# Performance work log

Hardware: AMD Instinct MI355X
Metric: run time of the kernel (lower is better)

The kernel has to match this reference:

```python
import jax, jax.numpy as jnp
import numpy as np

H = 512      # hidden_size
Z = 128      # z_dim
E = 512      # embedding_dim
D = 2 * H + Z  # GRU hidden / decoder state dim = 1152
V = 32000    # output_size
BS = 256
N = 128      # encoder nodes per source


def setup_inputs() -> dict:
    key = jax.random.key(0)
    ks = jax.random.split(key, 24)
    s = 0.05
    inp = {
        "prev_y": jax.random.normal(ks[0], (BS, E), jnp.float32),
        "prev_h": jax.random.normal(ks[1], (BS, D), jnp.float32),
        "equ_enc": jax.random.normal(ks[2], (BS, N, H), jnp.float32),
        "sns_enc": jax.random.normal(ks[3], (BS, N, H), jnp.float32),
        "z_sample": jax.random.normal(ks[4], (BS, Z), jnp.float32),
        "equ_mask": jax.random.randint(ks[5], (BS, N), 0, 2) > 0,
        "sns_mask": jax.random.randint(ks[6], (BS, N), 0, 2) > 0,
        # Attention (equ): W1: HxH, W2: HxD, vt: 1xH (torch Linear weight = [out,in])
        "W1e": jax.random.normal(ks[7], (H, H), jnp.float32) * s,
        "W2e": jax.random.normal(ks[8], (H, D), jnp.float32) * s,
        "vte": jax.random.normal(ks[9], (1, H), jnp.float32) * s,
        "W1s": jax.random.normal(ks[10], (H, H), jnp.float32) * s,
        "W2s": jax.random.normal(ks[11], (H, D), jnp.float32) * s,
        "vts": jax.random.normal(ks[12], (1, H), jnp.float32) * s,
        "plan_W": jax.random.normal(ks[13], (2, D), jnp.float32) * s,
        "plan_b": jax.random.normal(ks[14], (2,), jnp.float32) * s,
        "Wc": jax.random.normal(ks[15], (H, E + H), jnp.float32) * s,
        "bc": jax.random.normal(ks[16], (H,), jnp.float32) * s,
        # GRU: input H -> hidden D
        "w_ih": jax.random.normal(ks[17], (3 * D, H), jnp.float32) * s,
        "w_hh": jax.random.normal(ks[18], (3 * D, D), jnp.float32) * s,
        "b_ih": jax.random.normal(ks[19], (3 * D,), jnp.float32) * s,
        "b_hh": jax.random.normal(ks[20], (3 * D,), jnp.float32) * s,
        "Wout": jax.random.normal(ks[21], (V, D), jnp.float32) * s,
        "bout": jax.random.normal(ks[22], (V,), jnp.float32) * s,
    }
    return inp


def _attn(h, enc, mask, W1, W2, vt):
    # enc: (b,n,H), h: (b,D)
    et = jnp.einsum('bnh,kh->bnk', enc, W1)          # (b,n,H)
    dt = (h @ W2.T)[:, None, :]                       # (b,1,H)
    u = jnp.einsum('bnh,h->bn', jnp.tanh(et + dt), vt[0])
    u = jnp.where(mask, -jnp.inf, u)
    return jax.nn.softmax(u, axis=-1)                 # (b,n)


def reference(prev_y, prev_h, equ_enc, sns_enc, z_sample, equ_mask, sns_mask,
              W1e, W2e, vte, W1s, W2s, vts, plan_W, plan_b, Wc, bc,
              w_ih, w_hh, b_ih, b_hh, Wout, bout):
    aw_e = _attn(prev_h, equ_enc, equ_mask, W1e, W2e, vte)
    ctx_e = jnp.einsum('bn,bnh->bh', aw_e, equ_enc)
    aw_s = _attn(prev_h, sns_enc, sns_mask, W1s, W2s, vts)
    ctx_s = jnp.einsum('bn,bnh->bh', aw_s, sns_enc)
    plan = jax.nn.softmax(prev_h @ plan_W.T + plan_b, axis=-1)  # (b,2)
    combine = jnp.stack([ctx_e, ctx_s], axis=1)                  # (b,2,H)
    context = jnp.einsum('bk,bkh->bh', plan, combine)
    y_ctx = jnp.concatenate([prev_y, context], axis=-1)          # (b,E+H)
    x = y_ctx @ Wc.T + bc                                        # (b,H)
    # single-step GRU (torch gate order: r, z, n)
    gx = x @ w_ih.T + b_ih                                       # (b,3D)
    gh = prev_h @ w_hh.T + b_hh
    Dh = prev_h.shape[-1]
    gx_r, gx_z, gx_n = gx[:, :Dh], gx[:, Dh:2*Dh], gx[:, 2*Dh:]
    gh_r, gh_z, gh_n = gh[:, :Dh], gh[:, Dh:2*Dh], gh[:, 2*Dh:]
    r = jax.nn.sigmoid(gx_r + gh_r)
    zg = jax.nn.sigmoid(gx_z + gh_z)
    n = jnp.tanh(gx_n + r * gh_n)
    h_new = (1.0 - zg) * n + zg * prev_h                          # (b,D)
    dec_output = (h_new @ Wout.T + bout)[:, None, :]              # (b,1,V)
    dec_hidden = h_new[None]                                      # (1,b,D)
    return dec_output, dec_hidden, plan
```

## Files before the change

kernel.cpp:

```cpp
#include <hip/hip_runtime.h>
#include <stdint.h>
#include <math.h>

#define BS_  256
#define NSEQ 128
#define HH   512
#define DD   1152
#define VV   32000
#define BN_  (BS_*NSEQ)

typedef float  f32x4  __attribute__((ext_vector_type(4)));
typedef __bf16 bf16x8 __attribute__((ext_vector_type(8)));

__device__ __forceinline__ f32x4 mfma16(bf16x8 a, bf16x8 b, f32x4 c) {
    return __builtin_amdgcn_mfma_f32_16x16x32_bf16(a, b, c, 0, 0, 0);
}

__device__ __forceinline__ bf16x8 pack8(f32x4 a, f32x4 b) {
    bf16x8 v;
    v[0] = (__bf16)a[0]; v[1] = (__bf16)a[1]; v[2] = (__bf16)a[2]; v[3] = (__bf16)a[3];
    v[4] = (__bf16)b[0]; v[5] = (__bf16)b[1]; v[6] = (__bf16)b[2]; v[7] = (__bf16)b[3];
    return v;
}

__device__ __forceinline__ float tanh_fast(float x) {
    float e = __expf(2.f * x);
    return 1.f - __fdividef(2.f, e + 1.f);
}

__global__ __launch_bounds__(256) void k_tile128(
    const float* __restrict__ A, const float* __restrict__ B,
    const float* __restrict__ bias, float* __restrict__ C,
    int K, int ldc)
{
    const int rb = blockIdx.x * 128;
    const int cb = blockIdx.y * 128;
    const int t = threadIdx.x;
    const int w = t >> 6, wr = w >> 1, wc = w & 1;
    const int lane = t & 63, g = lane >> 4, r = lane & 15;
    const int s_row = t >> 1, s_h = t & 1;

    __shared__ bf16x8 sm[2][2][512];

    const float* Ap = A + (size_t)(rb + s_row) * K + s_h * 16;
    const float* Bp = B + (size_t)(cb + s_row) * K + s_h * 16;

    const int kg0 = 2 * s_h, kg1 = 2 * s_h + 1;
    const int swz0 = kg0 * 128 + ((s_row & 112) | ((s_row ^ (kg0 << 2)) & 15));
    const int swz1 = kg1 * 128 + ((s_row & 112) | ((s_row ^ (kg1 << 2)) & 15));

    int ai[4], bi[4];
    #pragma unroll
    for (int i = 0; i < 4; ++i) {
        ai[i] = g * 128 + wr * 64 + i * 16 + ((r ^ (g << 2)) & 15);
        bi[i] = g * 128 + wc * 64 + i * 16 + ((r ^ (g << 2)) & 15);
    }

    const int KS = K >> 5;
    f32x4 pa0 = ((const f32x4*)Ap)[0], pa1 = ((const f32x4*)Ap)[1],
          pa2 = ((const f32x4*)Ap)[2], pa3 = ((const f32x4*)Ap)[3];
    f32x4 pb0 = ((const f32x4*)Bp)[0], pb1 = ((const f32x4*)Bp)[1],
          pb2 = ((const f32x4*)Bp)[2], pb3 = ((const f32x4*)Bp)[3];

    f32x4 acc[4][4];
    #pragma unroll
    for (int i = 0; i < 4; ++i)
        #pragma unroll
        for (int j = 0; j < 4; ++j) acc[i][j] = (f32x4){0.f, 0.f, 0.f, 0.f};

    for (int kb = 0; kb < KS; ++kb) {
        const int buf = kb & 1;
        sm[buf][0][swz0] = pack8(pa0, pa1);
        sm[buf][0][swz1] = pack8(pa2, pa3);
        sm[buf][1][swz0] = pack8(pb0, pb1);
        sm[buf][1][swz1] = pack8(pb2, pb3);
        __syncthreads();
        if (kb + 1 < KS) {
            const float* a2 = Ap + (kb + 1) * 32;
            const float* b2 = Bp + (kb + 1) * 32;
            pa0 = ((const f32x4*)a2)[0]; pa1 = ((const f32x4*)a2)[1];
            pa2 = ((const f32x4*)a2)[2]; pa3 = ((const f32x4*)a2)[3];
            pb0 = ((const f32x4*)b2)[0]; pb1 = ((const f32x4*)b2)[1];
            pb2 = ((const f32x4*)b2)[2]; pb3 = ((const f32x4*)b2)[3];
        }
        bf16x8 af[4], bfr[4];
        #pragma unroll
        for (int i = 0; i < 4; ++i) af[i]  = sm[buf][0][ai[i]];
        #pragma unroll
        for (int j = 0; j < 4; ++j) bfr[j] = sm[buf][1][bi[j]];
        #pragma unroll
        for (int i = 0; i < 4; ++i)
            #pragma unroll
            for (int j = 0; j < 4; ++j)
                acc[i][j] = mfma16(af[i], bfr[j], acc[i][j]);
    }

    #pragma unroll
    for (int j = 0; j < 4; ++j) {
        const int col = cb + wc * 64 + j * 16 + r;
        const float bv = bias ? bias[col] : 0.f;
        #pragma unroll
        for (int i = 0; i < 4; ++i) {
            #pragma unroll
            for (int q = 0; q < 4; ++q) {
                const int row = rb + wr * 64 + i * 16 + g * 4 + q;
                C[(size_t)row * ldc + col] = acc[i][j][q] + bv;
            }
        }
    }
}

__global__ __launch_bounds__(256) void k_vocab(
    const float* __restrict__ A, const float* __restrict__ B,
    const float* __restrict__ bias, float* __restrict__ C,
    int K, int ldc)
{
    const int L = blockIdx.x;
    const int p  = (L & 7) + ((L >> 4) << 3);
    const int rr = (L >> 3) & 1;
    if (p >= 250) return;
    const int rb = rr * 128;
    const int cb = p * 128;

    const int t = threadIdx.x;
    const int w = t >> 6, wr = w >> 1, wc = w & 1;
    const int lane = t & 63, g = lane >> 4, r = lane & 15;
    const int s_row = t >> 1, s_h = t & 1;

    __shared__ bf16x8 sm[2][2][512];

    const float* Ap = A + (size_t)(rb + s_row) * K + s_h * 16;
    const float* Bp = B + (size_t)(cb + s_row) * K + s_h * 16;

    const int kg0 = 2 * s_h, kg1 = 2 * s_h + 1;
    const int swz0 = kg0 * 128 + ((s_row & 112) | ((s_row ^ (kg0 << 2)) & 15));
    const int swz1 = kg1 * 128 + ((s_row & 112) | ((s_row ^ (kg1 << 2)) & 15));

    int ai[4], bi[4];
    #pragma unroll
    for (int i = 0; i < 4; ++i) {
        ai[i] = g * 128 + wr * 64 + i * 16 + ((r ^ (g << 2)) & 15);
        bi[i] = g * 128 + wc * 64 + i * 16 + ((r ^ (g << 2)) & 15);
    }

    const int KS = K >> 5;
    f32x4 pa0 = ((const f32x4*)Ap)[0], pa1 = ((const f32x4*)Ap)[1],
          pa2 = ((const f32x4*)Ap)[2], pa3 = ((const f32x4*)Ap)[3];
    f32x4 pb0 = ((const f32x4*)Bp)[0], pb1 = ((const f32x4*)Bp)[1],
          pb2 = ((const f32x4*)Bp)[2], pb3 = ((const f32x4*)Bp)[3];

    f32x4 acc[4][4];
    #pragma unroll
    for (int i = 0; i < 4; ++i)
        #pragma unroll
        for (int j = 0; j < 4; ++j) acc[i][j] = (f32x4){0.f, 0.f, 0.f, 0.f};

    for (int kb = 0; kb < KS; ++kb) {
        const int buf = kb & 1;
        sm[buf][0][swz0] = pack8(pa0, pa1);
        sm[buf][0][swz1] = pack8(pa2, pa3);
        sm[buf][1][swz0] = pack8(pb0, pb1);
        sm[buf][1][swz1] = pack8(pb2, pb3);
        __syncthreads();
        if (kb + 1 < KS) {
            const float* a2 = Ap + (kb + 1) * 32;
            const float* b2 = Bp + (kb + 1) * 32;
            pa0 = ((const f32x4*)a2)[0]; pa1 = ((const f32x4*)a2)[1];
            pa2 = ((const f32x4*)a2)[2]; pa3 = ((const f32x4*)a2)[3];
            pb0 = ((const f32x4*)b2)[0]; pb1 = ((const f32x4*)b2)[1];
            pb2 = ((const f32x4*)b2)[2]; pb3 = ((const f32x4*)b2)[3];
        }
        bf16x8 af[4], bfr[4];
        #pragma unroll
        for (int i = 0; i < 4; ++i) af[i]  = sm[buf][0][ai[i]];
        #pragma unroll
        for (int j = 0; j < 4; ++j) bfr[j] = sm[buf][1][bi[j]];
        #pragma unroll
        for (int i = 0; i < 4; ++i)
            #pragma unroll
            for (int j = 0; j < 4; ++j)
                acc[i][j] = mfma16(af[i], bfr[j], acc[i][j]);
    }

    #pragma unroll
    for (int j = 0; j < 4; ++j) {
        const int col = cb + wc * 64 + j * 16 + r;
        const float bv = bias[col];
        #pragma unroll
        for (int i = 0; i < 4; ++i) {
            #pragma unroll
            for (int q = 0; q < 4; ++q) {
                const int row = rb + wr * 64 + i * 16 + g * 4 + q;
                C[(size_t)row * ldc + col] = acc[i][j][q] + bv;
            }
        }
    }
}

__global__ __launch_bounds__(256) void k_prevh(
    const float* __restrict__ prev_h, const float* __restrict__ W2e,
    const float* __restrict__ W2s, const float* __restrict__ w_hh,
    const float* __restrict__ b_hh,
    float* __restrict__ dt_e, float* __restrict__ dt_s, float* __restrict__ gh)
{
    const int cb = blockIdx.x * 64;
    const int rb = blockIdx.y * 64;
    const int t  = threadIdx.x;
    const int w = t >> 6, lane = t & 63, g = lane >> 4, r = lane & 15;
    const int s_row = t >> 2, s_kc = t & 3;
    const int K = DD;

    __shared__ bf16x8 sm[2][2][256];

    const float* Ap = prev_h + (size_t)(rb + s_row) * K + s_kc * 8;
    const float* Bp;
    {
        int brow = cb + s_row;
        if (cb < 512)        Bp = W2e + (size_t)brow * K;
        else if (cb < 1024)  Bp = W2s + (size_t)(brow - 512) * K;
        else                 Bp = w_hh + (size_t)(brow - 1024) * K;
        Bp += s_kc * 8;
    }

    const int KS = K >> 5;
    f32x4 pa0 = *(const f32x4*)Ap, pa1 = *(const f32x4*)(Ap + 4);
    f32x4 pb0 = *(const f32x4*)Bp, pb1 = *(const f32x4*)(Bp + 4);

    f32x4 acc[4] = {{0,0,0,0},{0,0,0,0},{0,0,0,0},{0,0,0,0}};

    for (int kb = 0; kb < KS; ++kb) {
        sm[kb & 1][0][s_kc * 64 + s_row] = pack8(pa0, pa1);
        sm[kb & 1][1][s_kc * 64 + s_row] = pack8(pb0, pb1);
        __syncthreads();
        if (kb + 1 < KS) {
            const float* a2 = Ap + (kb + 1) * 32;
            const float* b2 = Bp + (kb + 1) * 32;
            pa0 = *(const f32x4*)a2; pa1 = *(const f32x4*)(a2 + 4);
            pb0 = *(const f32x4*)b2; pb1 = *(const f32x4*)(b2 + 4);
        }
        bf16x8 af = sm[kb & 1][0][g * 64 + w * 16 + r];
        #pragma unroll
        for (int j = 0; j < 4; ++j) {
            bf16x8 bf = sm[kb & 1][1][g * 64 + j * 16 + r];
            acc[j] = mfma16(af, bf, acc[j]);
        }
    }

    #pragma unroll
    for (int j = 0; j < 4; ++j) {
        int col = cb + j * 16 + r;
        #pragma unroll
        for (int q = 0; q < 4; ++q) {
            int row = rb + w * 16 + g * 4 + q;
            float v = acc[j][q];
            if (cb < 512)       dt_e[(size_t)row * 512 + col] = v;
            else if (cb < 1024) dt_s[(size_t)row * 512 + (col - 512)] = v;
            else {
                int c0 = col - 1024;
                gh[(size_t)row * 3456 + c0] = v + b_hh[c0];
            }
        }
    }
}

__global__ __launch_bounds__(256) void k_attn(
    const float* __restrict__ enc_e, const float* __restrict__ enc_s,
    const float* __restrict__ W1e, const float* __restrict__ W1s,
    const float* __restrict__ vte, const float* __restrict__ vts,
    const float* __restrict__ dt_e, const float* __restrict__ dt_s,
    float* __restrict__ u_part)
{
    const int L = blockIdx.x;
    const int n = (L >> 3) & 3;
    const int G = (L & 7) + ((L >> 5) << 3);
    const int e = G >> 8;
    const int b = G & 255;

    const float* enc = e ? enc_s : enc_e;
    const float* W1  = e ? W1s  : W1e;
    const float* vt  = e ? vts  : vte;
    const float* dt  = e ? dt_s : dt_e;

    __shared__ bf16x8 sm[2][2][512];
    __shared__ float upart[2][128];

    const int t = threadIdx.x;
    const int w = t >> 6, wr = w >> 1, wc = w & 1;
    const int lane = t & 63, g = lane >> 4, r = lane & 15;
    const int s_row = t >> 1, s_h = t & 1;

    const int kg0 = 2 * s_h, kg1 = 2 * s_h + 1;
    const int swz0 = kg0 * 128 + ((s_row & 112) | ((s_row ^ (kg0 << 2)) & 15));
    const int swz1 = kg1 * 128 + ((s_row & 112) | ((s_row ^ (kg1 << 2)) & 15));

    int ai[4], bi[4];
    #pragma unroll
    for (int i = 0; i < 4; ++i) {
        ai[i] = g * 128 + wr * 64 + i * 16 + ((r ^ (g << 2)) & 15);
        bi[i] = g * 128 + wc * 64 + i * 16 + ((r ^ (g << 2)) & 15);
    }

    const float* Ap = enc + (size_t)(b * 128 + s_row) * 512 + s_h * 16;
    const float* Bp = W1 + (size_t)(n * 128 + s_row) * 512 + s_h * 16;

    f32x4 pa0 = ((const f32x4*)Ap)[0], pa1 = ((const f32x4*)Ap)[1],
          pa2 = ((const f32x4*)Ap)[2], pa3 = ((const f32x4*)Ap)[3];
    f32x4 pb0 = ((const f32x4*)Bp)[0], pb1 = ((const f32x4*)Bp)[1],
          pb2 = ((const f32x4*)Bp)[2], pb3 = ((const f32x4*)Bp)[3];

    f32x4 acc[4][4];
    #pragma unroll
    for (int i = 0; i < 4; ++i)
        #pragma unroll
        for (int j = 0; j < 4; ++j) acc[i][j] = (f32x4){0.f, 0.f, 0.f, 0.f};

    for (int kb = 0; kb < 16; ++kb) {
        const int buf = kb & 1;
        sm[buf][0][swz0] = pack8(pa0, pa1);
        sm[buf][0][swz1] = pack8(pa2, pa3);
        sm[buf][1][swz0] = pack8(pb0, pb1);
        sm[buf][1][swz1] = pack8(pb2, pb3);
        __syncthreads();
        if (kb + 1 < 16) {
            const float* a2 = Ap + (kb + 1) * 32;
            const float* b2 = Bp + (kb + 1) * 32;
            pa0 = ((const f32x4*)a2)[0]; pa1 = ((const f32x4*)a2)[1];
            pa2 = ((const f32x4*)a2)[2]; pa3 = ((const f32x4*)a2)[3];
            pb0 = ((const f32x4*)b2)[0]; pb1 = ((const f32x4*)b2)[1];
            pb2 = ((const f32x4*)b2)[2]; pb3 = ((const f32x4*)b2)[3];
        }
        bf16x8 af[4], bfr[4];
        #pragma unroll
        for (int i = 0; i < 4; ++i) af[i]  = sm[buf][0][ai[i]];
        #pragma unroll
        for (int j = 0; j < 4; ++j) bfr[j] = sm[buf][1][bi[j]];
        #pragma unroll
        for (int i = 0; i < 4; ++i)
            #pragma unroll
            for (int j = 0; j < 4; ++j)
                acc[i][j] = mfma16(af[i], bfr[j], acc[i][j]);
    }

    float dv[4], vv[4];
    #pragma unroll
    for (int j = 0; j < 4; ++j) {
        int col = n * 128 + wc * 64 + j * 16 + r;
        dv[j] = dt[(size_t)b * 512 + col];
        vv[j] = vt[col];
    }
    #pragma unroll
    for (int i = 0; i < 4; ++i) {
        #pragma unroll
        for (int q = 0; q < 4; ++q) {
            float s = 0.f;
            #pragma unroll
            for (int j = 0; j < 4; ++j)
                s += vv[j] * tanh_fast(acc[i][j][q] + dv[j]);
            #pragma unroll
            for (int m = 1; m < 16; m <<= 1) s += __shfl_xor(s, m);
            if (r == 0) upart[wc][wr * 64 + i * 16 + g * 4 + q] = s;
        }
    }
    __syncthreads();
    if (t < 128)
        u_part[((size_t)(n * 2 + e)) * BN_ + b * 128 + t] = upart[0][t] + upart[1][t];
}

__global__ __launch_bounds__(256) void k_ctx(
    const float* __restrict__ u_part, const int* __restrict__ mask_e,
    const int* __restrict__ mask_s, const float* __restrict__ enc_e,
    const float* __restrict__ enc_s, const float* __restrict__ prev_h,
    const float* __restrict__ plan_W, const float* __restrict__ plan_b,
    const float* __restrict__ prev_y,
    float* __restrict__ y_ctx, float* __restrict__ plan_out)
{
    const int b = blockIdx.x;
    const int rh = blockIdx.y;
    const int t = threadIdx.x;
    const int lane = t & 63, wid = t >> 6, half = t >> 7, n = t & 127;

    __shared__ float aw[2][128];
    __shared__ float red[16];
    __shared__ float planv[2];

    const int* mask = half ? mask_s : mask_e;
    float uv = u_part[(size_t)(0 * 2 + half) * BN_ + b * 128 + n]
             + u_part[(size_t)(1 * 2 + half) * BN_ + b * 128 + n]
             + u_part[(size_t)(2 * 2 + half) * BN_ + b * 128 + n]
             + u_part[(size_t)(3 * 2 + half) * BN_ + b * 128 + n];
    bool msk = mask[b * 128 + n] != 0;
    float val = msk ? -3.4e38f : uv;

    float mx = val;
    #pragma unroll
    for (int m = 1; m < 64; m <<= 1) mx = fmaxf(mx, __shfl_xor(mx, m));
    if (lane == 0) red[wid] = mx;
    __syncthreads();
    mx = fmaxf(red[half * 2], red[half * 2 + 1]);
    float ex = msk ? 0.f : __expf(uv - mx);
    float sm = ex;
    #pragma unroll
    for (int m = 1; m < 64; m <<= 1) sm += __shfl_xor(sm, m);
    if (lane == 0) red[4 + wid] = sm;
    __syncthreads();
    sm = red[4 + half * 2] + red[4 + half * 2 + 1];
    aw[half][n] = ex / sm;

    float p0 = 0.f, p1 = 0.f;
    for (int i = t; i < DD; i += 256) {
        float hv = prev_h[(size_t)b * DD + i];
        p0 += hv * plan_W[i];
        p1 += hv * plan_W[DD + i];
    }
    #pragma unroll
    for (int m = 1; m < 64; m <<= 1) { p0 += __shfl_xor(p0, m); p1 += __shfl_xor(p1, m); }
    if (lane == 0) { red[8 + wid] = p0; red[12 + wid] = p1; }
    __syncthreads();
    if (t == 0) {
        float l0 = red[8] + red[9] + red[10] + red[11] + plan_b[0];
        float l1 = red[12] + red[13] + red[14] + red[15] + plan_b[1];
        float mm = fmaxf(l0, l1);
        float e0 = __expf(l0 - mm), e1 = __expf(l1 - mm);
        float ss = e0 + e1;
        planv[0] = e0 / ss; planv[1] = e1 / ss;
        if (rh == 0) {
            plan_out[b * 2 + 0] = planv[0];
            plan_out[b * 2 + 1] = planv[1];
        }
    }
    __syncthreads();

    const int ee = t >> 7;
    const int tt = t & 127;
    const float pl = planv[ee];
    const float* base = (ee ? enc_s : enc_e) + (size_t)b * 65536 + (size_t)(rh * 64) * 512 + tt * 4;
    f32x4 accv = {0.f, 0.f, 0.f, 0.f};
    #pragma unroll 4
    for (int row = 0; row < 64; ++row) {
        f32x4 v = *(const f32x4*)(base + (size_t)row * 512);
        float a = aw[ee][rh * 64 + row];
        accv += a * v;
    }
    float* dst = y_ctx + (size_t)b * 1024 + 512 + tt * 4;
    atomicAdd(dst + 0, pl * accv[0]);
    atomicAdd(dst + 1, pl * accv[1]);
    atomicAdd(dst + 2, pl * accv[2]);
    atomicAdd(dst + 3, pl * accv[3]);

    if (rh == 0 && t < 128) {
        f32x4 v = *(const f32x4*)(prev_y + (size_t)b * 512 + t * 4);
        *(f32x4*)(y_ctx + (size_t)b * 1024 + t * 4) = v;
    }
}

__global__ __launch_bounds__(256) void k_gemm_bias(
    const float* __restrict__ A, const float* __restrict__ B,
    const float* __restrict__ bias, float* __restrict__ C,
    int K, int ldc)
{
    const int cb = blockIdx.x * 64;
    const int rb = blockIdx.y * 64;
    const int t  = threadIdx.x;
    const int w = t >> 6, lane = t & 63, g = lane >> 4, r = lane & 15;
    const int s_row = t >> 2, s_kc = t & 3;

    __shared__ bf16x8 sm[2][2][256];

    const float* Ap = A + (size_t)(rb + s_row) * K + s_kc * 8;
    const float* Bp = B + (size_t)(cb + s_row) * K + s_kc * 8;

    const int KS = K >> 5;
    f32x4 pa0 = *(const f32x4*)Ap, pa1 = *(const f32x4*)(Ap + 4);
    f32x4 pb0 = *(const f32x4*)Bp, pb1 = *(const f32x4*)(Bp + 4);

    f32x4 acc[4] = {{0,0,0,0},{0,0,0,0},{0,0,0,0},{0,0,0,0}};

    for (int kb = 0; kb < KS; ++kb) {
        sm[kb & 1][0][s_kc * 64 + s_row] = pack8(pa0, pa1);
        sm[kb & 1][1][s_kc * 64 + s_row] = pack8(pb0, pb1);
        __syncthreads();
        if (kb + 1 < KS) {
            const float* a2 = Ap + (kb + 1) * 32;
            const float* b2 = Bp + (kb + 1) * 32;
            pa0 = *(const f32x4*)a2; pa1 = *(const f32x4*)(a2 + 4);
            pb0 = *(const f32x4*)b2; pb1 = *(const f32x4*)(b2 + 4);
        }
        bf16x8 af = sm[kb & 1][0][g * 64 + w * 16 + r];
        #pragma unroll
        for (int j = 0; j < 4; ++j) {
            bf16x8 bf = sm[kb & 1][1][g * 64 + j * 16 + r];
            acc[j] = mfma16(af, bf, acc[j]);
        }
    }
    #pragma unroll
    for (int j = 0; j < 4; ++j) {
        int col = cb + j * 16 + r;
        float bv = bias ? bias[col] : 0.f;
        #pragma unroll
        for (int q = 0; q < 4; ++q) {
            int row = rb + w * 16 + g * 4 + q;
            C[(size_t)row * ldc + col] = acc[j][q] + bv;
        }
    }
}

__global__ __launch_bounds__(384) void k_gru(
    const float* __restrict__ gx, const float* __restrict__ gh,
    const float* __restrict__ prev_h, float* __restrict__ h_new,
    float* __restrict__ out_hidden)
{
    int d = blockIdx.x * 384 + threadIdx.x;
    int b = blockIdx.y;
    size_t o3 = (size_t)b * 3456;
    float xr = gx[o3 + d], xz = gx[o3 + 1152 + d], xn = gx[o3 + 2304 + d];
    float hr = gh[o3 + d], hz = gh[o3 + 1152 + d], hn = gh[o3 + 2304 + d];
    float rr = 1.f / (1.f + __expf(-(xr + hr)));
    float zz = 1.f / (1.f + __expf(-(xz + hz)));
    float nv = tanhf(xn + rr * hn);
    float hv = (1.f - zz) * nv + zz * prev_h[(size_t)b * DD + d];
    h_new[(size_t)b * DD + d] = hv;
    out_hidden[(size_t)b * DD + d] = hv;
}

extern "C" void kernel_launch(void* const* d_in, const int* in_sizes, int n_in,
                              void* d_out, int out_size, void* d_ws, size_t ws_size,
                              hipStream_t stream)
{
    const float* prev_y = (const float*)d_in[0];
    const float* prev_h = (const float*)d_in[1];
    const float* enc_e  = (const float*)d_in[2];
    const float* enc_s  = (const float*)d_in[3];
    const int*   mask_e = (const int*)d_in[5];
    const int*   mask_s = (const int*)d_in[6];
    const float* W1e    = (const float*)d_in[7];
    const float* W2e    = (const float*)d_in[8];
    const float* vte    = (const float*)d_in[9];
    const float* W1s    = (const float*)d_in[10];
    const float* W2s    = (const float*)d_in[11];
    const float* vts    = (const float*)d_in[12];
    const float* plan_W = (const float*)d_in[13];
    const float* plan_b = (const float*)d_in[14];
    const float* Wc     = (const float*)d_in[15];
    const float* bc     = (const float*)d_in[16];
    const float* w_ih   = (const float*)d_in[17];
    const float* w_hh   = (const float*)d_in[18];
    const float* b_ih   = (const float*)d_in[19];
    const float* b_hh   = (const float*)d_in[20];
    const float* Wout   = (const float*)d_in[21];
    const float* bout   = (const float*)d_in[22];

    float* out = (float*)d_out;
    float* ws  = (float*)d_ws;

    float* gh     = ws;
    float* big2   = ws + 884736;
    float* upxx   = big2 + 884736;
    float* y_ctx  = upxx + 262144;
    float* h_new  = y_ctx + 262144;

    float* dt_e  = big2;
    float* dt_s  = big2 + 131072;
    float* gx    = big2;
    float* u_part = upxx;
    float* xx    = upxx;

    float* dec_out  = out;
    float* dec_hid  = out + 8192000;
    float* plan_out = out + 8486912;

    hipMemsetAsync(y_ctx, 0, 262144 * sizeof(float), stream);

    k_prevh<<<dim3(70, 4), 256, 0, stream>>>(prev_h, W2e, W2s, w_hh, b_hh,
                                             dt_e, dt_s, gh);

    k_attn<<<dim3(2048), 256, 0, stream>>>(
        enc_e, enc_s, W1e, W1s, vte, vts, dt_e, dt_s, u_part);

    k_ctx<<<dim3(BS_, 2), 256, 0, stream>>>(u_part, mask_e, mask_s, enc_e, enc_s,
                                            prev_h, plan_W, plan_b, prev_y,
                                            y_ctx, plan_out);

    k_gemm_bias<<<dim3(8, 4), 256, 0, stream>>>(y_ctx, Wc, bc, xx, 1024, 512);
    k_tile128<<<dim3(2, 27), 256, 0, stream>>>(xx, w_ih, b_ih, gx, 512, 3456);

    k_gru<<<dim3(3, BS_), 384, 0, stream>>>(gx, gh, prev_h, h_new, dec_hid);

    k_vocab<<<dim3(512), 256, 0, stream>>>(h_new, Wout, bout, dec_out,
                                           1152, 32000);
}
```

Baseline: 550.2 us.

## Use async global-to-LDS loads and pre-cast bf16 operands in attention and vocab GEMMs

Rewrites the attention and vocab GEMM kernels to fetch tiles with global_load_lds directly into XOR-swizzled shared memory. The bf16 conversion of the fp32 side now happens when fragments are read from LDS. The small operands (W1e/W1s and h_new) are pre-cast to bf16 by a new cast kernel or by the GRU kernel, which halves their load bytes. The aim is to remove register-staged prefetch and store-to-LDS overhead and overlap loads with MFMA. The cost is two extra cast launches per call, and fp32 tiles in LDS double shared-memory use for the large operand.

```diff
diff --git a/kernel.cpp b/kernel.cpp
--- a/kernel.cpp
+++ b/kernel.cpp
@@ -26,6 +26,230 @@
 __device__ __forceinline__ float tanh_fast(float x) {
     float e = __expf(2.f * x);
     return 1.f - __fdividef(2.f, e + 1.f);
+}
+
+__device__ __forceinline__ void gload16(const void* g, void* l) {
+    __builtin_amdgcn_global_load_lds(
+        (const __attribute__((address_space(1))) void*)g,
+        (__attribute__((address_space(3))) void*)l, 16, 0, 0);
+}
+
+__global__ __launch_bounds__(256) void k_cast(const float* __restrict__ src,
+                                              __bf16* __restrict__ dst, int n8)
+{
+    int i = blockIdx.x * 256 + threadIdx.x;
+    int stride = gridDim.x * 256;
+    for (; i < n8; i += stride) {
+        const f32x4* s = (const f32x4*)(src + (size_t)i * 8);
+        f32x4 a = s[0], b = s[1];
+        *(bf16x8*)(dst + (size_t)i * 8) = pack8(a, b);
+    }
+}
+
+__global__ __launch_bounds__(256) void k_attn2(
+    const float* __restrict__ enc_e, const float* __restrict__ enc_s,
+    const __bf16* __restrict__ W1be, const __bf16* __restrict__ W1bs,
+    const float* __restrict__ vte, const float* __restrict__ vts,
+    const float* __restrict__ dt_e, const float* __restrict__ dt_s,
+    float* __restrict__ u_part)
+{
+    const int L = blockIdx.x;
+    const int n = (L >> 3) & 3;
+    const int G = (L & 7) + ((L >> 5) << 3);
+    const int e = G >> 8;
+    const int b = G & 255;
+
+    const float*  enc = e ? enc_s : enc_e;
+    const __bf16* W1  = e ? W1bs : W1be;
+    const float*  vt  = e ? vts : vte;
+    const float*  dt  = e ? dt_s : dt_e;
+
+    __shared__ float  lA[2][4096];
+    __shared__ __bf16 lB[2][4096];
+    __shared__ float  upart[2][128];
+
+    const int t = threadIdx.x;
+    const int w = t >> 6, wr = w >> 1, wc = w & 1;
+    const int lane = t & 63, g = lane >> 4, r = lane & 15;
+
+    const float*  Ag = enc + (size_t)b * (128 * 512);
+    const __bf16* Bg = W1 + (size_t)n * (128 * 512);
+
+    int aoff[4], boff[2], aldsb[4], bldsb[2];
+    #pragma unroll
+    for (int i = 0; i < 4; ++i) {
+        int c = i * 256 + w * 64 + lane;
+        int row = c >> 3, kc = c & 7;
+        aoff[i]  = row * 512 + ((kc ^ (row & 7)) << 2);
+        aldsb[i] = (i * 256 + w * 64) << 2;
+    }
+    #pragma unroll
+    for (int i = 0; i < 2; ++i) {
+        int c = i * 256 + w * 64 + lane;
+        int row = c >> 2, kc = c & 3;
+        boff[i]  = row * 512 + ((kc ^ ((row >> 1) & 3)) << 3);
+        bldsb[i] = (i * 256 + w * 64) << 3;
+    }
+
+    f32x4 acc[4][4];
+    #pragma unroll
+    for (int i = 0; i < 4; ++i)
+        #pragma unroll
+        for (int j = 0; j < 4; ++j) acc[i][j] = (f32x4){0.f, 0.f, 0.f, 0.f};
+
+    #pragma unroll
+    for (int i = 0; i < 4; ++i) gload16(Ag + aoff[i], &lA[0][aldsb[i]]);
+    #pragma unroll
+    for (int i = 0; i < 2; ++i) gload16(Bg + boff[i], &lB[0][bldsb[i]]);
+
+    for (int kb = 0; kb < 16; ++kb) {
+        const int buf = kb & 1;
+        __syncthreads();
+        if (kb + 1 < 16) {
+            const int k0 = (kb + 1) * 32;
+            #pragma unroll
+            for (int i = 0; i < 4; ++i) gload16(Ag + aoff[i] + k0, &lA[buf ^ 1][aldsb[i]]);
+            #pragma unroll
+            for (int i = 0; i < 2; ++i) gload16(Bg + boff[i] + k0, &lB[buf ^ 1][bldsb[i]]);
+        }
+        bf16x8 af[4], bfr[4];
+        #pragma unroll
+        for (int j = 0; j < 4; ++j) {
+            int row = wc * 64 + j * 16 + r;
+            bfr[j] = *(const bf16x8*)&lB[buf][row * 32 + ((g ^ ((row >> 1) & 3)) << 3)];
+        }
+        #pragma unroll
+        for (int i = 0; i < 4; ++i) {
+            int row = wr * 64 + i * 16 + r;
+            int s = row & 7;
+            f32x4 a0 = *(const f32x4*)&lA[buf][row * 32 + (((g << 1) ^ s) << 2)];
+            f32x4 a1 = *(const f32x4*)&lA[buf][row * 32 + ((((g << 1) | 1) ^ s) << 2)];
+            af[i] = pack8(a0, a1);
+        }
+        #pragma unroll
+        for (int i = 0; i < 4; ++i)
+            #pragma unroll
+            for (int j = 0; j < 4; ++j)
+                acc[i][j] = mfma16(af[i], bfr[j], acc[i][j]);
+    }
+
+    float dv[4], vv[4];
+    #pragma unroll
+    for (int j = 0; j < 4; ++j) {
+        int col = n * 128 + wc * 64 + j * 16 + r;
+        dv[j] = dt[(size_t)b * 512 + col];
+        vv[j] = vt[col];
+    }
+    #pragma unroll
+    for (int i = 0; i < 4; ++i) {
+        #pragma unroll
+        for (int q = 0; q < 4; ++q) {
+            float s = 0.f;
+            #pragma unroll
+            for (int j = 0; j < 4; ++j)
+                s += vv[j] * tanh_fast(acc[i][j][q] + dv[j]);
+            #pragma unroll
+            for (int m = 1; m < 16; m <<= 1) s += __shfl_xor(s, m);
+            if (r == 0) upart[wc][wr * 64 + i * 16 + g * 4 + q] = s;
+        }
+    }
+    __syncthreads();
+    if (t < 128)
+        u_part[((size_t)(n * 2 + e)) * BN_ + b * 128 + t] = upart[0][t] + upart[1][t];
+}
+
+__global__ __launch_bounds__(256) void k_vocab2(
+    const __bf16* __restrict__ A,
+    const float* __restrict__ B,
+    const float* __restrict__ bias, float* __restrict__ C)
+{
+    const int L = blockIdx.x;
+    const int p  = (L & 7) + ((L >> 4) << 3);
+    const int rr = (L >> 3) & 1;
+    if (p >= 250) return;
+    const int rb = rr * 128, cb = p * 128;
+
+    __shared__ __bf16 lA[2][4096];
+    __shared__ float  lB[2][4096];
+
+    const int t = threadIdx.x;
+    const int w = t >> 6, wr = w >> 1, wc = w & 1;
+    const int lane = t & 63, g = lane >> 4, r = lane & 15;
+
+    const __bf16* Ag = A + (size_t)rb * DD;
+    const float*  Bg = B + (size_t)cb * DD;
+
+    int aoff[2], boff[4], aldsb[2], bldsb[4];
+    #pragma unroll
+    for (int i = 0; i < 2; ++i) {
+        int c = i * 256 + w * 64 + lane;
+        int row = c >> 2, kc = c & 3;
+        aoff[i]  = row * DD + ((kc ^ ((row >> 1) & 3)) << 3);
+        aldsb[i] = (i * 256 + w * 64) << 3;
+    }
+    #pragma unroll
+    for (int i = 0; i < 4; ++i) {
+        int c = i * 256 + w * 64 + lane;
+        int row = c >> 3, kc = c & 7;
+        boff[i]  = row * DD + ((kc ^ (row & 7)) << 2);
+        bldsb[i] = (i * 256 + w * 64) << 2;
+    }
+
+    f32x4 acc[4][4];
+    #pragma unroll
+    for (int i = 0; i < 4; ++i)
+        #pragma unroll
+        for (int j = 0; j < 4; ++j) acc[i][j] = (f32x4){0.f, 0.f, 0.f, 0.f};
+
+    #pragma unroll
+    for (int i = 0; i < 2; ++i) gload16(Ag + aoff[i], &lA[0][aldsb[i]]);
+    #pragma unroll
+    for (int i = 0; i < 4; ++i) gload16(Bg + boff[i], &lB[0][bldsb[i]]);
+
+    for (int kb = 0; kb < 36; ++kb) {
+        const int buf = kb & 1;
+        __syncthreads();
+        if (kb + 1 < 36) {
+            const int k0 = (kb + 1) * 32;
+            #pragma unroll
+            for (int i = 0; i < 2; ++i) gload16(Ag + aoff[i] + k0, &lA[buf ^ 1][aldsb[i]]);
+            #pragma unroll
+            for (int i = 0; i < 4; ++i) gload16(Bg + boff[i] + k0, &lB[buf ^ 1][bldsb[i]]);
+        }
+        bf16x8 af[4], bfr[4];
+        #pragma unroll
+        for (int i = 0; i < 4; ++i) {
+            int row = wr * 64 + i * 16 + r;
+            af[i] = *(const bf16x8*)&lA[buf][row * 32 + ((g ^ ((row >> 1) & 3)) << 3)];
+        }
+        #pragma unroll
+        for (int j = 0; j < 4; ++j) {
+            int row = wc * 64 + j * 16 + r;
+            int s = row & 7;
+            f32x4 b0 = *(const f32x4*)&lB[buf][row * 32 + (((g << 1) ^ s) << 2)];
+            f32x4 b1 = *(const f32x4*)&lB[buf][row * 32 + ((((g << 1) | 1) ^ s) << 2)];
+            bfr[j] = pack8(b0, b1);
+        }
+        #pragma unroll
+        for (int i = 0; i < 4; ++i)
+            #pragma unroll
+            for (int j = 0; j < 4; ++j)
+                acc[i][j] = mfma16(af[i], bfr[j], acc[i][j]);
+    }
+
+    #pragma unroll
+    for (int j = 0; j < 4; ++j) {
+        const int col = cb + wc * 64 + j * 16 + r;
+        const float bv = bias[col];
+        #pragma unroll
+        for (int i = 0; i < 4; ++i) {
+            #pragma unroll
+            for (int q = 0; q < 4; ++q) {
+                const int row = rb + wr * 64 + i * 16 + g * 4 + q;
+                C[(size_t)row * VV + col] = acc[i][j][q] + bv;
+            }
+        }
+    }
 }
 
 __global__ __launch_bounds__(256) void k_tile128(
@@ -110,93 +334,6 @@
     }
 }
 
-__global__ __launch_bounds__(256) void k_vocab(
-    const float* __restrict__ A, const float* __restrict__ B,
-    const float* __restrict__ bias, float* __restrict__ C,
-    int K, int ldc)
-{
-    const int L = blockIdx.x;
-    const int p  = (L & 7) + ((L >> 4) << 3);
-    const int rr = (L >> 3) & 1;
-    if (p >= 250) return;
-    const int rb = rr * 128;
-    const int cb = p * 128;
-
-    const int t = threadIdx.x;
-    const int w = t >> 6, wr = w >> 1, wc = w & 1;
-    const int lane = t & 63, g = lane >> 4, r = lane & 15;
-    const int s_row = t >> 1, s_h = t & 1;
-
-    __shared__ bf16x8 sm[2][2][512];
-
-    const float* Ap = A + (size_t)(rb + s_row) * K + s_h * 16;
-    const float* Bp = B + (size_t)(cb + s_row) * K + s_h * 16;
-
-    const int kg0 = 2 * s_h, kg1 = 2 * s_h + 1;
-    const int swz0 = kg0 * 128 + ((s_row & 112) | ((s_row ^ (kg0 << 2)) & 15));
-    const int swz1 = kg1 * 128 + ((s_row & 112) | ((s_row ^ (kg1 << 2)) & 15));
-
-    int ai[4], bi[4];
-    #pragma unroll
-    for (int i = 0; i < 4; ++i) {
-        ai[i] = g * 128 + wr * 64 + i * 16 + ((r ^ (g << 2)) & 15);
-        bi[i] = g * 128 + wc * 64 + i * 16 + ((r ^ (g << 2)) & 15);
-    }
-
-    const int KS = K >> 5;
-    f32x4 pa0 = ((const f32x4*)Ap)[0], pa1 = ((const f32x4*)Ap)[1],
-          pa2 = ((const f32x4*)Ap)[2], pa3 = ((const f32x4*)Ap)[3];
-    f32x4 pb0 = ((const f32x4*)Bp)[0], pb1 = ((const f32x4*)Bp)[1],
-          pb2 = ((const f32x4*)Bp)[2], pb3 = ((const f32x4*)Bp)[3];
-
-    f32x4 acc[4][4];
-    #pragma unroll
-    for (int i = 0; i < 4; ++i)
-        #pragma unroll
-        for (int j = 0; j < 4; ++j) acc[i][j] = (f32x4){0.f, 0.f, 0.f, 0.f};
-
-    for (int kb = 0; kb < KS; ++kb) {
-        const int buf = kb & 1;
-        sm[buf][0][swz0] = pack8(pa0, pa1);
-        sm[buf][0][swz1] = pack8(pa2, pa3);
-        sm[buf][1][swz0] = pack8(pb0, pb1);
-        sm[buf][1][swz1] = pack8(pb2, pb3);
-        __syncthreads();
-        if (kb + 1 < KS) {
-            const float* a2 = Ap + (kb + 1) * 32;
-            const float* b2 = Bp + (kb + 1) * 32;
-            pa0 = ((const f32x4*)a2)[0]; pa1 = ((const f32x4*)a2)[1];
-            pa2 = ((const f32x4*)a2)[2]; pa3 = ((const f32x4*)a2)[3];
-            pb0 = ((const f32x4*)b2)[0]; pb1 = ((const f32x4*)b2)[1];
-            pb2 = ((const f32x4*)b2)[2]; pb3 = ((const f32x4*)b2)[3];
-        }
-        bf16x8 af[4], bfr[4];
-        #pragma unroll
-        for (int i = 0; i < 4; ++i) af[i]  = sm[buf][0][ai[i]];
-        #pragma unroll
-        for (int j = 0; j < 4; ++j) bfr[j] = sm[buf][1][bi[j]];
-        #pragma unroll
-        for (int i = 0; i < 4; ++i)
-            #pragma unroll
-            for (int j = 0; j < 4; ++j)
-                acc[i][j] = mfma16(af[i], bfr[j], acc[i][j]);
-    }
-
-    #pragma unroll
-    for (int j = 0; j < 4; ++j) {
-        const int col = cb + wc * 64 + j * 16 + r;
-        const float bv = bias[col];
-        #pragma unroll
-        for (int i = 0; i < 4; ++i) {
-            #pragma unroll
-            for (int q = 0; q < 4; ++q) {
-                const int row = rb + wr * 64 + i * 16 + g * 4 + q;
-                C[(size_t)row * ldc + col] = acc[i][j][q] + bv;
-            }
-        }
-    }
-}
-
 __global__ __launch_bounds__(256) void k_prevh(
     const float* __restrict__ prev_h, const float* __restrict__ W2e,
     const float* __restrict__ W2s, const float* __restrict__ w_hh,
@@ -261,109 +398,6 @@
             }
         }
     }
-}
-
-__global__ __launch_bounds__(256) void k_attn(
-    const float* __restrict__ enc_e, const float* __restrict__ enc_s,
-    const float* __restrict__ W1e, const float* __restrict__ W1s,
-    const float* __restrict__ vte, const float* __restrict__ vts,
-    const float* __restrict__ dt_e, const float* __restrict__ dt_s,
-    float* __restrict__ u_part)
-{
-    const int L = blockIdx.x;
-    const int n = (L >> 3) & 3;
-    const int G = (L & 7) + ((L >> 5) << 3);
-    const int e = G >> 8;
-    const int b = G & 255;
-
-    const float* enc = e ? enc_s : enc_e;
-    const float* W1  = e ? W1s  : W1e;
-    const float* vt  = e ? vts  : vte;
-    const float* dt  = e ? dt_s : dt_e;
-
-    __shared__ bf16x8 sm[2][2][512];
-    __shared__ float upart[2][128];
-
-    const int t = threadIdx.x;
-    const int w = t >> 6, wr = w >> 1, wc = w & 1;
-    const int lane = t & 63, g = lane >> 4, r = lane & 15;
-    const int s_row = t >> 1, s_h = t & 1;
-
-    const int kg0 = 2 * s_h, kg1 = 2 * s_h + 1;
-    const int swz0 = kg0 * 128 + ((s_row & 112) | ((s_row ^ (kg0 << 2)) & 15));
-    const int swz1 = kg1 * 128 + ((s_row & 112) | ((s_row ^ (kg1 << 2)) & 15));
-
-    int ai[4], bi[4];
-    #pragma unroll
-    for (int i = 0; i < 4; ++i) {
-        ai[i] = g * 128 + wr * 64 + i * 16 + ((r ^ (g << 2)) & 15);
-        bi[i] = g * 128 + wc * 64 + i * 16 + ((r ^ (g << 2)) & 15);
-    }
-
-    const float* Ap = enc + (size_t)(b * 128 + s_row) * 512 + s_h * 16;
-    const float* Bp = W1 + (size_t)(n * 128 + s_row) * 512 + s_h * 16;
-
-    f32x4 pa0 = ((const f32x4*)Ap)[0], pa1 = ((const f32x4*)Ap)[1],
-          pa2 = ((const f32x4*)Ap)[2], pa3 = ((const f32x4*)Ap)[3];
-    f32x4 pb0 = ((const f32x4*)Bp)[0], pb1 = ((const f32x4*)Bp)[1],
-          pb2 = ((const f32x4*)Bp)[2], pb3 = ((const f32x4*)Bp)[3];
-
-    f32x4 acc[4][4];
-    #pragma unroll
-    for (int i = 0; i < 4; ++i)
-        #pragma unroll
-        for (int j = 0; j < 4; ++j) acc[i][j] = (f32x4){0.f, 0.f, 0.f, 0.f};
-
-    for (int kb = 0; kb < 16; ++kb) {
-        const int buf = kb & 1;
-        sm[buf][0][swz0] = pack8(pa0, pa1);
-        sm[buf][0][swz1] = pack8(pa2, pa3);
-        sm[buf][1][swz0] = pack8(pb0, pb1);
-        sm[buf][1][swz1] = pack8(pb2, pb3);
-        __syncthreads();
-        if (kb + 1 < 16) {
-            const float* a2 = Ap + (kb + 1) * 32;
-            const float* b2 = Bp + (kb + 1) * 32;
-            pa0 = ((const f32x4*)a2)[0]; pa1 = ((const f32x4*)a2)[1];
-            pa2 = ((const f32x4*)a2)[2]; pa3 = ((const f32x4*)a2)[3];
-            pb0 = ((const f32x4*)b2)[0]; pb1 = ((const f32x4*)b2)[1];
-            pb2 = ((const f32x4*)b2)[2]; pb3 = ((const f32x4*)b2)[3];
-        }
-        bf16x8 af[4], bfr[4];
-        #pragma unroll
-        for (int i = 0; i < 4; ++i) af[i]  = sm[buf][0][ai[i]];
-        #pragma unroll
-        for (int j = 0; j < 4; ++j) bfr[j] = sm[buf][1][bi[j]];
-        #pragma unroll
-        for (int i = 0; i < 4; ++i)
-            #pragma unroll
-            for (int j = 0; j < 4; ++j)
-                acc[i][j] = mfma16(af[i], bfr[j], acc[i][j]);
-    }
-
-    float dv[4], vv[4];
-    #pragma unroll
-    for (int j = 0; j < 4; ++j) {
-        int col = n * 128 + wc * 64 + j * 16 + r;
-        dv[j] = dt[(size_t)b * 512 + col];
-        vv[j] = vt[col];
-    }
-    #pragma unroll
-    for (int i = 0; i < 4; ++i) {
-        #pragma unroll
-        for (int q = 0; q < 4; ++q) {
-            float s = 0.f;
-            #pragma unroll
-            for (int j = 0; j < 4; ++j)
-                s += vv[j] * tanh_fast(acc[i][j][q] + dv[j]);
-            #pragma unroll
-            for (int m = 1; m < 16; m <<= 1) s += __shfl_xor(s, m);
-            if (r == 0) upart[wc][wr * 64 + i * 16 + g * 4 + q] = s;
-        }
-    }
-    __syncthreads();
-    if (t < 128)
-        u_part[((size_t)(n * 2 + e)) * BN_ + b * 128 + t] = upart[0][t] + upart[1][t];
 }
 
 __global__ __launch_bounds__(256) void k_ctx(
@@ -507,7 +541,7 @@
 __global__ __launch_bounds__(384) void k_gru(
     const float* __restrict__ gx, const float* __restrict__ gh,
     const float* __restrict__ prev_h, float* __restrict__ h_new,
-    float* __restrict__ out_hidden)
+    float* __restrict__ out_hidden, __bf16* __restrict__ h_new_bf)
 {
     int d = blockIdx.x * 384 + threadIdx.x;
     int b = blockIdx.y;
@@ -520,6 +554,7 @@
     float hv = (1.f - zz) * nv + zz * prev_h[(size_t)b * DD + d];
     h_new[(size_t)b * DD + d] = hv;
     out_hidden[(size_t)b * DD + d] = hv;
+    h_new_bf[(size_t)b * DD + d] = (__bf16)hv;
 }
 
 extern "C" void kernel_launch(void* const* d_in, const int* in_sizes, int n_in,
@@ -557,6 +592,9 @@
     float* upxx   = big2 + 884736;
     float* y_ctx  = upxx + 262144;
     float* h_new  = y_ctx + 262144;
+    __bf16* W1be  = (__bf16*)(h_new + 294912);
+    __bf16* W1bs  = W1be + 262144;
+    __bf16* hnbf  = W1bs + 262144;
 
     float* dt_e  = big2;
     float* dt_s  = big2 + 131072;
@@ -570,11 +608,14 @@
 
     hipMemsetAsync(y_ctx, 0, 262144 * sizeof(float), stream);
 
+    k_cast<<<dim3(128), 256, 0, stream>>>(W1e, W1be, 32768);
+    k_cast<<<dim3(128), 256, 0, stream>>>(W1s, W1bs, 32768);
+
     k_prevh<<<dim3(70, 4), 256, 0, stream>>>(prev_h, W2e, W2s, w_hh, b_hh,
                                              dt_e, dt_s, gh);
 
-    k_attn<<<dim3(2048), 256, 0, stream>>>(
-        enc_e, enc_s, W1e, W1s, vte, vts, dt_e, dt_s, u_part);
+    k_attn2<<<dim3(2048), 256, 0, stream>>>(
+        enc_e, enc_s, W1be, W1bs, vte, vts, dt_e, dt_s, u_part);
 
     k_ctx<<<dim3(BS_, 2), 256, 0, stream>>>(u_part, mask_e, mask_s, enc_e, enc_s,
                                             prev_h, plan_W, plan_b, prev_y,
@@ -583,8 +624,7 @@
     k_gemm_bias<<<dim3(8, 4), 256, 0, stream>>>(y_ctx, Wc, bc, xx, 1024, 512);
     k_tile128<<<dim3(2, 27), 256, 0, stream>>>(xx, w_ih, b_ih, gx, 512, 3456);
 
-    k_gru<<<dim3(3, BS_), 384, 0, stream>>>(gx, gh, prev_h, h_new, dec_hid);
-
-    k_vocab<<<dim3(512), 256, 0, stream>>>(h_new, Wout, bout, dec_out,
-                                           1152, 32000);
-}
+    k_gru<<<dim3(3, BS_), 384, 0, stream>>>(gx, gh, prev_h, h_new, dec_hid, hnbf);
+
+    k_vocab2<<<dim3(512), 256, 0, stream>>>(hnbf, Wout, bout, dec_out);
+}
```

Result: slower. 579.4 us (+5.3%).
